# Kernel optimization log

Measured on AMD Instinct MI355X. Metric: run time of the kernel, lower is better.

## Reference

```python
import jax, jax.numpy as jnp
import numpy as np

W_BITS = 4  # active precision (max of supported_bits)
EPS = 0.005  # clamp margin from the original module


def _dequant_kbit(qweight, lut, w_bits):
    """Bit-plane LUT dequant.
    qweight: [w_bits, O, I//32] int32, plane b holds bit b (MSB-first code) of each
    weight's k-bit index, 32 consecutive input positions per int32 word (LSB-first
    within a word). lut: [O, 2**w_bits]. Returns dense weight [O, I].
    """
    O = qweight.shape[1]
    shifts = jnp.arange(32, dtype=jnp.int32)                     # bit position within word
    bits = (qweight[:, :, :, None] >> shifts) & 1                # [w_bits, O, I//32, 32]
    plane_w = (1 << (w_bits - 1 - jnp.arange(w_bits, dtype=jnp.int32)))
    idx = (bits * plane_w[:, None, None, None]).sum(axis=0)      # [O, I//32, 32]
    idx = idx.reshape(O, -1)                                     # [O, I]
    return jnp.take_along_axis(lut, idx, axis=1)                 # [O, I]


def _csr_dense(rows, cols, vals, O, I):
    """Scatter CSR (indptr=rows) into a dense [O, I] matrix."""
    nnz = cols.shape[0]
    k = jnp.arange(nnz, dtype=rows.dtype)
    row_ids = jnp.searchsorted(rows, k, side='right') - 1        # CSR row of each nnz
    return jnp.zeros((O, I), dtype=vals.dtype).at[row_ids, cols].add(vals)


def setup_inputs() -> dict:
    key = jax.random.key(0)
    ks = jax.random.split(key, 7)
    B, S, I, O = 4, 2048, 4096, 4096
    NNZ = 65536
    x = jax.random.normal(ks[0], (B, S, I), dtype=jnp.float32)
    qweight = jax.random.randint(ks[1], (W_BITS, O, I // 32), 0, 2147483647, dtype=jnp.int32)
    lut = jax.random.normal(ks[2], (O, 2 ** W_BITS), dtype=jnp.float32) * 0.05
    rows = jnp.sort(jax.random.randint(ks[3], (O + 1,), 0, NNZ, dtype=jnp.int32))
    rows = rows.at[0].set(0).at[-1].set(NNZ)                     # valid CSR indptr
    cols = jax.random.randint(ks[4], (NNZ,), 0, I, dtype=jnp.int32)
    vals = jax.random.normal(ks[5], (NNZ,), dtype=jnp.float32) * 0.01
    bias = jax.random.normal(ks[6], (O,), dtype=jnp.float32) * 0.01
    return {"x": x, "qweight": qweight, "lut": lut, "rows": rows,
            "cols": cols, "vals": vals, "bias": bias}


def reference(x, qweight, lut, rows, cols, vals, bias):
    O = qweight.shape[1]
    I = x.shape[-1]
    weight = _dequant_kbit(qweight, lut, W_BITS)                 # [O, I]
    y = jnp.einsum('bsi,oi->bso', x, weight)                     # dense quantized GEMM
    w_sp = _csr_dense(rows, cols, vals, O, I)                    # sparse outlier weights
    y = y + jnp.einsum('bsi,oi->bso', x, w_sp)
    y = y + bias
    fmax = jnp.finfo(x.dtype).max * (1.0 - EPS)
    return jnp.clip(y, -fmax, fmax)
```

## Files before the change

### kernel.cpp

```cpp
#include <hip/hip_runtime.h>
#include <stdint.h>

#define Mdim 8192
#define Ndim 4096
#define Kdim 4096

#define BM 256
#define BN 256
#define BK 32
#define NT (Kdim / BK)

typedef float f32x4 __attribute__((ext_vector_type(4)));
typedef __bf16 bf16x8 __attribute__((ext_vector_type(8)));
typedef unsigned short ushort_t;

#define FMAXC 3.3858093490333422e+38f

__device__ __forceinline__ ushort_t f2bf(float f) {
    unsigned u = __float_as_uint(f);
    u += 0x7fffu + ((u >> 16) & 1u);
    return (ushort_t)(u >> 16);
}

__device__ __forceinline__ void gload_lds16(const void* g, void* l) {
    __builtin_amdgcn_global_load_lds(
        (const __attribute__((address_space(1))) uint32_t*)g,
        (__attribute__((address_space(3))) uint32_t*)(uint32_t)(uintptr_t)l,
        16, 0, 0);
}

__global__ __launch_bounds__(128) void dequant_kernel(
        const int* __restrict__ qw, const float* __restrict__ lut,
        const int* __restrict__ rows, const int* __restrict__ cols,
        const float* __restrict__ vals, ushort_t* __restrict__ w16) {
    __shared__ float wrow[128 * 33];
    __shared__ float slut[16];
    const int o = blockIdx.x;
    const int t = threadIdx.x;

    if (t < 16) slut[t] = lut[o * 16 + t];
    __syncthreads();

    const int q0 = qw[0 * Ndim * 128 + o * 128 + t];
    const int q1 = qw[1 * Ndim * 128 + o * 128 + t];
    const int q2 = qw[2 * Ndim * 128 + o * 128 + t];
    const int q3 = qw[3 * Ndim * 128 + o * 128 + t];
    float* dst = &wrow[t * 33];
#pragma unroll
    for (int j = 0; j < 32; ++j) {
        int idx = (((q0 >> j) & 1) << 3) | (((q1 >> j) & 1) << 2) |
                  (((q2 >> j) & 1) << 1) | ((q3 >> j) & 1);
        dst[j] = slut[idx];
    }
    __syncthreads();

    const int beg = rows[o], end = rows[o + 1];
    for (int k = beg + t; k < end; k += 128) {
        int c = cols[k];
        atomicAdd(&wrow[c + (c >> 5)], vals[k]);
    }
    __syncthreads();

    __align__(16) ushort_t tmp[32];
#pragma unroll
    for (int j = 0; j < 32; ++j) tmp[j] = f2bf(dst[j]);
    uint4* dstg = (uint4*)(w16 + (size_t)o * Kdim + t * 32);
    const uint4* srcg = (const uint4*)tmp;
#pragma unroll
    for (int j = 0; j < 4; ++j) dstg[j] = srcg[j];
}

__global__ __launch_bounds__(256) void convx_kernel(
        const float* __restrict__ x, ushort_t* __restrict__ y) {
    size_t i = ((size_t)blockIdx.x * 256 + threadIdx.x) * 8;
    float4 a = *(const float4*)(x + i);
    float4 b = *(const float4*)(x + i + 4);
    __align__(16) ushort_t r[8] = {f2bf(a.x), f2bf(a.y), f2bf(a.z), f2bf(a.w),
                                   f2bf(b.x), f2bf(b.y), f2bf(b.z), f2bf(b.w)};
    *(uint4*)(y + i) = *(const uint4*)r;
}

__global__ __launch_bounds__(512, 2) void gemm_kernel(
        const ushort_t* __restrict__ A, const ushort_t* __restrict__ Bw,
        const float* __restrict__ bias, float* __restrict__ C) {
    __shared__ __align__(16) char lds[131072];

    const int wgid = blockIdx.x;
    const int swz = (wgid & 7) * 64 + (wgid >> 3);
    const int bn = swz & 15, bm = swz >> 4;
    const int m0 = bm * BM, n0 = bn * BN;

    const int tid = threadIdx.x;
    const int lane = tid & 63, wid = tid >> 6;
    const int wr = wid >> 2, wc = wid & 3;
    const int fr = lane & 15, kg = lane >> 4;

    const int sline = tid >> 3;
    const int slot = (tid & 7) ^ (sline & 7);
    const int srow0 = (sline << 1) + (slot >> 2);
    const int skel = (slot & 3) * 8;
    const ushort_t* gA = A + (size_t)(m0 + srow0) * Kdim + skel;
    const ushort_t* gB = Bw + (size_t)(n0 + srow0) * Kdim + skel;

    const int offL = (fr >> 1) * 128 + (((((fr & 1) << 2) | kg) ^ (fr >> 1)) << 4);

    f32x4 acc[8][4];
#pragma unroll
    for (int i = 0; i < 8; ++i)
#pragma unroll
        for (int j = 0; j < 4; ++j) acc[i][j] = (f32x4){0.f, 0.f, 0.f, 0.f};

    const ushort_t* pA = gA;
    const ushort_t* pB = gB;

    auto stageA = [&](int bufd) {
        char* d = lds + bufd * 16384 + tid * 16;
        gload_lds16(pA, d);
        gload_lds16(pA + (size_t)128 * Kdim, d + 8192);
    };
    auto stageB = [&](int bufd) {
        char* d = lds + 65536 + bufd * 16384 + tid * 16;
        gload_lds16(pB, d);
        gload_lds16(pB + (size_t)128 * Kdim, d + 8192);
    };
    auto readFrags = [&](bf16x8 (&FA)[8], bf16x8 (&FB)[4], int bufidx) {
        const char* Ab = lds + bufidx * 16384;
        const char* Bb = lds + 65536 + bufidx * 16384;
#pragma unroll
        for (int n = 0; n < 4; ++n) {
            FA[n] = *(const bf16x8*)(Ab + wr * 8192 + n * 1024 + offL);
            FB[n] = *(const bf16x8*)(Bb + wc * 4096 + n * 1024 + offL);
        }
#pragma unroll
        for (int m = 4; m < 8; ++m)
            FA[m] = *(const bf16x8*)(Ab + wr * 8192 + m * 1024 + offL);
    };
    auto mfmaTile = [&](bf16x8 (&FA)[8], bf16x8 (&FB)[4]) {
        __builtin_amdgcn_s_setprio(1);
#pragma unroll
        for (int m = 0; m < 8; ++m)
#pragma unroll
            for (int n = 0; n < 4; ++n)
                acc[m][n] = __builtin_amdgcn_mfma_f32_16x16x32_bf16(
                    FA[m], FB[n], acc[m][n], 0, 0, 0);
        __builtin_amdgcn_s_setprio(0);
    };

    stageA(0); stageB(0); pA += BK; pB += BK;
    stageA(1); stageB(1); pA += BK; pB += BK;
    stageA(2); stageB(2); pA += BK; pB += BK;
    asm volatile("s_waitcnt vmcnt(4)" ::: "memory");
    asm volatile("s_barrier" ::: "memory");

    bf16x8 FAa[8], FAb[8];
    bf16x8 FBa[4], FBb[4];
    readFrags(FAa, FBa, 0);

#pragma unroll 1
    for (int t = 0; t < NT; t += 2) {
        readFrags(FAb, FBb, (t + 1) & 3);
        if (t + 3 < NT) { stageA((t + 3) & 3); stageB((t + 3) & 3); }
        pA += BK; pB += BK;
        mfmaTile(FAa, FBa);
        if (t < NT - 3) {
            asm volatile("s_waitcnt vmcnt(4)" ::: "memory");
        } else {
            asm volatile("s_waitcnt vmcnt(0)" ::: "memory");
        }
        asm volatile("s_barrier" ::: "memory");

        if (t + 2 < NT) readFrags(FAa, FBa, (t + 2) & 3);
        if (t + 4 < NT) { stageA((t + 4) & 3); stageB((t + 4) & 3); }
        pA += BK; pB += BK;
        mfmaTile(FAb, FBb);
        if (t + 1 < NT - 3) {
            asm volatile("s_waitcnt vmcnt(4)" ::: "memory");
        } else {
            asm volatile("s_waitcnt vmcnt(0)" ::: "memory");
        }
        asm volatile("s_barrier" ::: "memory");
    }

    const int rg = lane >> 4;
#pragma unroll
    for (int nf = 0; nf < 4; ++nf) {
        const int col = n0 + wc * 64 + nf * 16 + fr;
        const float bv = bias[col];
#pragma unroll
        for (int mf = 0; mf < 8; ++mf) {
            const int row = m0 + wr * 128 + mf * 16 + rg * 4;
            float* outp = C + (size_t)row * Ndim + col;
#pragma unroll
            for (int j = 0; j < 4; ++j) {
                float v = acc[mf][nf][j] + bv;
                v = fminf(fmaxf(v, -FMAXC), FMAXC);
                outp[(size_t)j * Ndim] = v;
            }
        }
    }
}

extern "C" void kernel_launch(void* const* d_in, const int* in_sizes, int n_in,
                              void* d_out, int out_size, void* d_ws, size_t ws_size,
                              hipStream_t stream) {
    const float* x    = (const float*)d_in[0];
    const int*   qw   = (const int*)d_in[1];
    const float* lut  = (const float*)d_in[2];
    const int*   rows = (const int*)d_in[3];
    const int*   cols = (const int*)d_in[4];
    const float* vals = (const float*)d_in[5];
    const float* bias = (const float*)d_in[6];
    float* out = (float*)d_out;

    ushort_t* x16 = (ushort_t*)d_ws;
    ushort_t* w16 = x16 + (size_t)Mdim * Kdim;

    hipLaunchKernelGGL(dequant_kernel, dim3(Ndim), dim3(128), 0, stream,
                       qw, lut, rows, cols, vals, w16);
    hipLaunchKernelGGL(convx_kernel, dim3((Mdim * Kdim) / (256 * 8)), dim3(256), 0, stream,
                       x, x16);
    hipLaunchKernelGGL(gemm_kernel, dim3((Mdim / BM) * (Ndim / BN)), dim3(512), 0, stream,
                       x16, w16, bias, out);
}
```

Before: 290.3 us.

## Interleave MFMAs with LDS reads and global loads via sched_group_barrier, peel tail

Adds sched_group_barrier groups so the compiler interleaves the 32 MFMAs of each half-step with the LDS fragment reads and global-to-LDS stage loads, instead of issuing them in separate blocks. The main loop's last iterations are peeled into an epilogue, which removes the per-iteration bounds checks and the conditional waitcnt selection. The asm waits drop their memory clobbers and are fenced with sched_barrier instead, and the s_setprio raising around the MFMAs is removed. The goal is better overlap of memory traffic with matrix math. It risks a worse schedule if the forced grouping does not match the actual instruction counts.

```diff
diff --git a/kernel.cpp b/kernel.cpp
--- a/kernel.cpp
+++ b/kernel.cpp
@@ -28,6 +28,8 @@
         (__attribute__((address_space(3))) uint32_t*)(uint32_t)(uintptr_t)l,
         16, 0, 0);
 }
+
+#define SGB(mask, n) __builtin_amdgcn_sched_group_barrier(mask, n, 0)
 
 __global__ __launch_bounds__(128) void dequant_kernel(
         const int* __restrict__ qw, const float* __restrict__ lut,
@@ -136,49 +138,73 @@
             FA[m] = *(const bf16x8*)(Ab + wr * 8192 + m * 1024 + offL);
     };
     auto mfmaTile = [&](bf16x8 (&FA)[8], bf16x8 (&FB)[4]) {
-        __builtin_amdgcn_s_setprio(1);
 #pragma unroll
         for (int m = 0; m < 8; ++m)
 #pragma unroll
             for (int n = 0; n < 4; ++n)
                 acc[m][n] = __builtin_amdgcn_mfma_f32_16x16x32_bf16(
                     FA[m], FB[n], acc[m][n], 0, 0, 0);
-        __builtin_amdgcn_s_setprio(0);
+    };
+    auto sgbHalf = [&]() {
+        SGB(0x30, 2); SGB(0x8, 2);
+        SGB(0x30, 2); SGB(0x8, 2);
+#pragma unroll
+        for (int i = 0; i < 12; ++i) { SGB(0x100, 1); SGB(0x8, 2); }
+        SGB(0x8, 4);
     };
 
     stageA(0); stageB(0); pA += BK; pB += BK;
     stageA(1); stageB(1); pA += BK; pB += BK;
     stageA(2); stageB(2); pA += BK; pB += BK;
-    asm volatile("s_waitcnt vmcnt(4)" ::: "memory");
-    asm volatile("s_barrier" ::: "memory");
+    asm volatile("s_waitcnt vmcnt(4)");
+    __builtin_amdgcn_sched_barrier(0);
+    __builtin_amdgcn_s_barrier();
 
     bf16x8 FAa[8], FAb[8];
     bf16x8 FBa[4], FBb[4];
     readFrags(FAa, FBa, 0);
 
 #pragma unroll 1
-    for (int t = 0; t < NT; t += 2) {
+    for (int t = 0; t < NT - 4; t += 2) {
         readFrags(FAb, FBb, (t + 1) & 3);
-        if (t + 3 < NT) { stageA((t + 3) & 3); stageB((t + 3) & 3); }
+        stageA((t + 3) & 3); stageB((t + 3) & 3);
         pA += BK; pB += BK;
         mfmaTile(FAa, FBa);
-        if (t < NT - 3) {
-            asm volatile("s_waitcnt vmcnt(4)" ::: "memory");
-        } else {
-            asm volatile("s_waitcnt vmcnt(0)" ::: "memory");
-        }
-        asm volatile("s_barrier" ::: "memory");
-
-        if (t + 2 < NT) readFrags(FAa, FBa, (t + 2) & 3);
-        if (t + 4 < NT) { stageA((t + 4) & 3); stageB((t + 4) & 3); }
+        sgbHalf();
+        asm volatile("s_waitcnt vmcnt(4)");
+        __builtin_amdgcn_sched_barrier(0);
+        __builtin_amdgcn_s_barrier();
+
+        readFrags(FAa, FBa, (t + 2) & 3);
+        stageA((t + 4) & 3); stageB((t + 4) & 3);
         pA += BK; pB += BK;
         mfmaTile(FAb, FBb);
-        if (t + 1 < NT - 3) {
-            asm volatile("s_waitcnt vmcnt(4)" ::: "memory");
-        } else {
-            asm volatile("s_waitcnt vmcnt(0)" ::: "memory");
-        }
-        asm volatile("s_barrier" ::: "memory");
+        sgbHalf();
+        asm volatile("s_waitcnt vmcnt(4)");
+        __builtin_amdgcn_sched_barrier(0);
+        __builtin_amdgcn_s_barrier();
+    }
+
+    {
+        readFrags(FAb, FBb, 125 & 3);
+        stageA(127 & 3); stageB(127 & 3);
+        mfmaTile(FAa, FBa);
+        sgbHalf();
+        asm volatile("s_waitcnt vmcnt(4)");
+        __builtin_amdgcn_sched_barrier(0);
+        __builtin_amdgcn_s_barrier();
+
+        readFrags(FAa, FBa, 126 & 3);
+        mfmaTile(FAb, FBb);
+        asm volatile("s_waitcnt vmcnt(0)");
+        __builtin_amdgcn_sched_barrier(0);
+        __builtin_amdgcn_s_barrier();
+    }
+
+    {
+        readFrags(FAb, FBb, 127 & 3);
+        mfmaTile(FAa, FBa);
+        mfmaTile(FAb, FBb);
     }
 
     const int rg = lane >> 4;
```

Result: faster. 282.1 us (-2.8%).
